# Optimization experiments

Hardware: AMD Instinct MI355X
Metric: run time of the kernel (lower is better)

## Reference

```python
import jax, jax.numpy as jnp
import numpy as np

N_QUBITS = 8
D_K = 64
B, S = 8, 1024


def _single_qubit_states(xang, theta):
    # xang: [B,S,n] values in [-1,1] (post-tanh); theta: [n,3] Rot params (phi, theta, omega)
    # state = RZ(omega) @ RY(th) @ RZ(phi) @ RY(pi*xang) |0>
    a = xang * jnp.pi
    c = jnp.cos(a * 0.5)          # [B,S,n]
    s = jnp.sin(a * 0.5)
    phi, th, om = theta[:, 0], theta[:, 1], theta[:, 2]   # each [n]
    ct = jnp.cos(th * 0.5)
    st = jnp.sin(th * 0.5)
    e_mpo = jnp.exp(-0.5j * (phi + om))   # e^{-i(phi+omega)/2}
    e_pmo = jnp.exp(0.5j * (phi - om))    # e^{+i(phi-omega)/2}
    amp0 = e_mpo * ct * c - e_pmo * st * s
    amp1 = jnp.conj(e_pmo) * st * c + jnp.conj(e_mpo) * ct * s
    return jnp.stack([amp0, amp1], axis=-1)   # [B,S,n,2] complex64


def setup_inputs() -> dict:
    key = jax.random.key(0)
    k1, k2, k3, k4 = jax.random.split(key, 4)
    x = jax.random.normal(k1, (B, S, D_K), dtype=jnp.float32)
    theta_q = jax.random.normal(k2, (N_QUBITS, 3), dtype=jnp.float32) * 0.1
    theta_k = jax.random.normal(k3, (N_QUBITS, 3), dtype=jnp.float32) * 0.1
    W_v = jax.random.normal(k4, (D_K, D_K), dtype=jnp.float32) / np.sqrt(D_K)
    b_v = jnp.zeros((D_K,), dtype=jnp.float32)
    return {"x": x, "theta_q": theta_q, "theta_k": theta_k, "W_v": W_v, "b_v": b_v}


def reference(x, theta_q, theta_k, W_v, b_v):
    n = theta_q.shape[0]
    xn = jnp.tanh(x[..., :n])                 # [B,S,n]
    qs = _single_qubit_states(xn, theta_q)    # [B,S,n,2]
    ks = _single_qubit_states(xn, theta_k)    # [B,S,n,2]
    # per-qubit overlap <q_i | k_j> for every (b, s, t) pair
    ov = jnp.einsum('bsnc,btnc->bstn', jnp.conj(qs), ks)  # [B,S,S,n] complex
    mag2 = jnp.real(ov) ** 2 + jnp.imag(ov) ** 2
    core = jnp.prod(mag2, axis=-1)            # |<psi_q|psi_k>|^2 = swap-test <Z>
    scores = (core + 1.0) * 0.5               # [B,S,S]
    attn = jax.nn.softmax(scores, axis=-1)
    values = x @ W_v.T + b_v                  # [B,S,D]
    out = jnp.einsum('bst,btd->bsd', attn, values)
    return out, attn
```

## Files before the change

### kernel.cpp

```cpp
#include <hip/hip_runtime.h>
#include <hip/hip_fp16.h>
#include <math.h>

#define NQ 8
#define DK 64
#define NB 8
#define NS 1024
#define RB 8
#define EPITCH 1032

typedef _Float16 h2v __attribute__((ext_vector_type(2)));

__device__ __forceinline__ float fdot2h(unsigned qu, unsigned ku, float acc) {
#if defined(__has_builtin) && __has_builtin(__builtin_amdgcn_fdot2)
    union { unsigned u; h2v h; } a, b;
    a.u = qu; b.u = ku;
    return __builtin_amdgcn_fdot2(a.h, b.h, acc, false);
#else
    __half2 qh = *(__half2*)&qu, kh = *(__half2*)&ku;
    float2 qf = __half22float2(qh), kf = __half22float2(kh);
    return fmaf(qf.x, kf.x, fmaf(qf.y, kf.y, acc));
#endif
}

__global__ __launch_bounds__(256) void prep_kernel(
    const float* __restrict__ x,
    const float* __restrict__ theta_q,
    const float* __restrict__ theta_k,
    const float* __restrict__ Wv,
    const float* __restrict__ bv,
    __half* __restrict__ qdh, __half* __restrict__ kdh,
    __half* __restrict__ v2) {
    int bid = blockIdx.x;
    int tid = threadIdx.x;
    if (bid < 2048) {
        int t = bid * 4 + (tid >> 6);
        int d = tid & 63;
        const float4* xr = (const float4*)(x + (size_t)t * DK);
        const float4* wr = (const float4*)(Wv + (size_t)d * DK);
        float a0 = bv[d], a1 = 0.f, a2 = 0.f, a3 = 0.f;
#pragma unroll
        for (int j = 0; j < DK / 4; ++j) {
            float4 xv = xr[j], wv = wr[j];
            a0 = fmaf(xv.x, wv.x, a0);
            a1 = fmaf(xv.y, wv.y, a1);
            a2 = fmaf(xv.z, wv.z, a2);
            a3 = fmaf(xv.w, wv.w, a3);
        }
        float v = (a0 + a1) + (a2 + a3);
        int b = t >> 10, ti = t & 1023;
        v2[((size_t)(b * 512 + (ti >> 1)) * 64 + d) * 2 + (ti & 1)] = __float2half_rn(v);
    } else {
        __shared__ float tt[2][NQ][6];
        if (tid < 16) {
            int side = tid >> 3, n = tid & 7;
            const float* thp = side ? theta_k : theta_q;
            float phi = thp[n * 3 + 0], th = thp[n * 3 + 1], om = thp[n * 3 + 2];
            float st, ct; __sincosf(0.5f * th, &st, &ct);
            float smpo, cmpo; __sincosf(0.5f * (phi + om), &smpo, &cmpo);
            float spmo, cpmo; __sincosf(0.5f * (phi - om), &spmo, &cpmo);
            tt[side][n][0] = ct;  tt[side][n][1] = st;
            tt[side][n][2] = cmpo; tt[side][n][3] = smpo;
            tt[side][n][4] = cpmo; tt[side][n][5] = spmo;
        }
        __syncthreads();

        int gid = (bid - 2048) * 256 + tid;
        int tok = gid >> 3;
        int n = gid & 7;
        float xin = x[(size_t)tok * DK + n];
        float ex = __expf(2.0f * xin);
        float xn = 1.0f - 2.0f / (ex + 1.0f);
        float s, c;
        __sincosf(xn * 1.57079632679489662f, &s, &c);

#pragma unroll
        for (int side = 0; side < 2; ++side) {
            float ct = tt[side][n][0], st = tt[side][n][1];
            float cmpo = tt[side][n][2], smpo = tt[side][n][3];
            float cpmo = tt[side][n][4], spmo = tt[side][n][5];
            float a = ct * c, b2 = st * s, cc = st * c, d2 = ct * s;
            float a0re =  cmpo * a - cpmo * b2;
            float a0im = -smpo * a - spmo * b2;
            float a1re =  cpmo * cc + cmpo * d2;
            float a1im = -spmo * cc + smpo * d2;
            float d0 = fmaf(a0re, a0re, a0im * a0im);
            float d1 = fmaf(a1re, a1re, a1im * a1im);
            float ur = fmaf(a1re, a0re, a1im * a0im);
            float ui = fmaf(a1im, a0re, -a1re * a0im);
            if (side == 0) {
                __half2* qp = (__half2*)(qdh + (size_t)tok * 32 + n * 4);
                qp[0] = __floats2half2_rn(d0, d1);
                qp[1] = __floats2half2_rn(ur, ui);
            } else {
                __half2* kp = (__half2*)(kdh + (size_t)tok * 32 + n * 4);
                kp[0] = __floats2half2_rn(d0, d1);
                kp[1] = __floats2half2_rn(2.f * ur, 2.f * ui);
            }
        }
    }
}

__global__ __launch_bounds__(256, 4) void attn_kernel(
    const __half* __restrict__ qdh, const __half* __restrict__ kdh,
    const __half* __restrict__ v2,
    float* __restrict__ out, float* __restrict__ attn) {
    __shared__ __align__(16) unsigned char smem[RB * EPITCH * 2];
    __half (*e16)[EPITCH] = (__half(*)[EPITCH])smem;
    float* red = (float*)smem;
    __shared__ float red_lds[4][RB];
    __shared__ float inv_lds[RB];

    int tid = threadIdx.x;
    int gr0 = blockIdx.x * RB;
    int b = gr0 >> 10;
    int w = tid >> 6, lane = tid & 63;

    const __half* kfb = kdh + (size_t)b * NS * 32;

    int t0 = w * 256;
    uint4 kv[4][4];
#pragma unroll
    for (int j = 0; j < 4; ++j) {
        const uint4* kp = (const uint4*)(kfb + (size_t)(t0 + j * 64 + lane) * 32);
        kv[j][0] = kp[0]; kv[j][1] = kp[1]; kv[j][2] = kp[2]; kv[j][3] = kp[3];
    }

    float sums[RB];
#pragma unroll
    for (int r = 0; r < RB; ++r) sums[r] = 0.f;

#pragma unroll
    for (int r = 0; r < RB; ++r) {
        const unsigned* qp = (const unsigned*)(qdh + (size_t)(gr0 + r) * 32);
        unsigned sq[16];
#pragma unroll
        for (int i = 0; i < 16; ++i) sq[i] = __builtin_amdgcn_readfirstlane(qp[i]);
#pragma unroll
        for (int j = 0; j < 4; ++j) {
            float m0 = fdot2h(sq[ 0], kv[j][0].x, fdot2h(sq[ 1], kv[j][0].y, 0.f));
            float m1 = fdot2h(sq[ 2], kv[j][0].z, fdot2h(sq[ 3], kv[j][0].w, 0.f));
            float m2 = fdot2h(sq[ 4], kv[j][1].x, fdot2h(sq[ 5], kv[j][1].y, 0.f));
            float m3 = fdot2h(sq[ 6], kv[j][1].z, fdot2h(sq[ 7], kv[j][1].w, 0.f));
            float m4 = fdot2h(sq[ 8], kv[j][2].x, fdot2h(sq[ 9], kv[j][2].y, 0.f));
            float m5 = fdot2h(sq[10], kv[j][2].z, fdot2h(sq[11], kv[j][2].w, 0.f));
            float m6 = fdot2h(sq[12], kv[j][3].x, fdot2h(sq[13], kv[j][3].y, 0.f));
            float m7 = fdot2h(sq[14], kv[j][3].z, fdot2h(sq[15], kv[j][3].w, 0.f));
            float core = ((m0 * m1) * (m2 * m3)) * ((m4 * m5) * (m6 * m7));
            float e = __expf(fmaf(core, 0.5f, 0.5f));
            e16[r][t0 + j * 64 + lane] = __float2half_rn(e);
            sums[r] += e;
        }
    }

#pragma unroll
    for (int r = 0; r < RB; ++r) {
#pragma unroll
        for (int m = 1; m < 64; m <<= 1) sums[r] += __shfl_xor(sums[r], m, 64);
    }
    if (lane == 0) {
#pragma unroll
        for (int r = 0; r < RB; ++r) red_lds[w][r] = sums[r];
    }
    __syncthreads();
    if (tid < RB)
        inv_lds[tid] = 1.f / (red_lds[0][tid] + red_lds[1][tid] + red_lds[2][tid] + red_lds[3][tid]);
    __syncthreads();

    float* ab = attn + (size_t)gr0 * NS;
#pragma unroll
    for (int r = 0; r < RB; ++r) {
        float iv = inv_lds[r];
        uint2 raw = *(const uint2*)&e16[r][tid * 4];
        __half2* hp = (__half2*)&raw;
        float2 lo = __half22float2(hp[0]), hi = __half22float2(hp[1]);
        *(float4*)&ab[(size_t)r * NS + tid * 4] =
            make_float4(lo.x * iv, lo.y * iv, hi.x * iv, hi.y * iv);
    }

    int tg = tid >> 4, dg = tid & 15;
    const __half* v2b = v2 + (size_t)b * 512 * 128;
    float acc[RB][4];
#pragma unroll
    for (int r = 0; r < RB; ++r) { acc[r][0] = acc[r][1] = acc[r][2] = acc[r][3] = 0.f; }

    for (int jj = 0; jj < 32; ++jj) {
        int p = jj * 16 + tg;
        uint4 vv = *(const uint4*)(v2b + (size_t)p * 128 + dg * 8);
        unsigned ep[RB];
#pragma unroll
        for (int r = 0; r < RB; ++r) ep[r] = *(const unsigned*)&e16[r][2 * p];
#pragma unroll
        for (int r = 0; r < RB; ++r) {
            acc[r][0] = fdot2h(ep[r], vv.x, acc[r][0]);
            acc[r][1] = fdot2h(ep[r], vv.y, acc[r][1]);
            acc[r][2] = fdot2h(ep[r], vv.z, acc[r][2]);
            acc[r][3] = fdot2h(ep[r], vv.w, acc[r][3]);
        }
    }

#pragma unroll
    for (int h = 0; h < 2; ++h) {
        __syncthreads();
#pragma unroll
        for (int r = 0; r < 4; ++r) {
            *(float4*)&red[((size_t)tg * 4 + r) * 64 + dg * 4] =
                make_float4(acc[h * 4 + r][0], acc[h * 4 + r][1],
                            acc[h * 4 + r][2], acc[h * 4 + r][3]);
        }
        __syncthreads();
        int r2 = tid >> 6, d = tid & 63;
        float o = 0.f;
#pragma unroll
        for (int g = 0; g < 16; ++g) o += red[((size_t)g * 4 + r2) * 64 + d];
        out[((size_t)(gr0 + h * 4 + r2)) * DK + d] = o * inv_lds[h * 4 + r2];
    }
}

extern "C" void kernel_launch(void* const* d_in, const int* in_sizes, int n_in,
                              void* d_out, int out_size, void* d_ws, size_t ws_size,
                              hipStream_t stream) {
    const float* x       = (const float*)d_in[0];
    const float* theta_q = (const float*)d_in[1];
    const float* theta_k = (const float*)d_in[2];
    const float* W_v     = (const float*)d_in[3];
    const float* b_v     = (const float*)d_in[4];

    float* out  = (float*)d_out;
    float* attn = (float*)d_out + (size_t)NB * NS * DK;

    __half* qdh = (__half*)d_ws;
    __half* kdh = qdh + (size_t)NB * NS * 32;
    __half* v2  = kdh + (size_t)NB * NS * 32;

    prep_kernel<<<2048 + NB * NS * NQ / 256, 256, 0, stream>>>(
        x, theta_q, theta_k, W_v, b_v, qdh, kdh, v2);
    attn_kernel<<<NB * NS / RB, 256, 0, stream>>>(qdh, kdh, v2, out, attn);
}
```

Measured before the change: 52.37 us.

## Fuse query state prep into attention kernel and pair tokens in value projection

The query density-matrix computation moves from the prep kernel into the attention kernel. Each block now builds the fp16 query terms for its 8 rows in shared memory, which removes the qdh workspace round trip. The value projection now computes two tokens per thread, so each W_v row is loaded once per pair and written as a single half2 store, and the block count drops by half. The V loop in the attention kernel prefetches the next vector before the dot products, at the cost of an extra barrier and some redundant per-block trig work.

```diff
diff --git a/kernel.cpp b/kernel.cpp
--- a/kernel.cpp
+++ b/kernel.cpp
@@ -23,91 +23,93 @@
 #endif
 }
 
+__device__ __forceinline__ void qk_density(float s, float c,
+                                           const float* t6,
+                                           float& d0, float& d1, float& ur, float& ui) {
+    float ct = t6[0], st = t6[1], cmpo = t6[2], smpo = t6[3], cpmo = t6[4], spmo = t6[5];
+    float a = ct * c, b2 = st * s, cc = st * c, d2 = ct * s;
+    float a0re =  cmpo * a - cpmo * b2;
+    float a0im = -smpo * a - spmo * b2;
+    float a1re =  cpmo * cc + cmpo * d2;
+    float a1im = -spmo * cc + smpo * d2;
+    d0 = fmaf(a0re, a0re, a0im * a0im);
+    d1 = fmaf(a1re, a1re, a1im * a1im);
+    ur = fmaf(a1re, a0re, a1im * a0im);
+    ui = fmaf(a1im, a0re, -a1re * a0im);
+}
+
+__device__ __forceinline__ void theta_table(const float* __restrict__ thp, int n, float* t6) {
+    float phi = thp[n * 3 + 0], th = thp[n * 3 + 1], om = thp[n * 3 + 2];
+    float st, ct; __sincosf(0.5f * th, &st, &ct);
+    float smpo, cmpo; __sincosf(0.5f * (phi + om), &smpo, &cmpo);
+    float spmo, cpmo; __sincosf(0.5f * (phi - om), &spmo, &cpmo);
+    t6[0] = ct; t6[1] = st; t6[2] = cmpo; t6[3] = smpo; t6[4] = cpmo; t6[5] = spmo;
+}
+
+__device__ __forceinline__ void tanh_sincos(float xin, float& s, float& c) {
+    float ex = __expf(2.0f * xin);
+    float xn = 1.0f - 2.0f / (ex + 1.0f);
+    __sincosf(xn * 1.57079632679489662f, &s, &c);
+}
+
 __global__ __launch_bounds__(256) void prep_kernel(
     const float* __restrict__ x,
-    const float* __restrict__ theta_q,
     const float* __restrict__ theta_k,
     const float* __restrict__ Wv,
     const float* __restrict__ bv,
-    __half* __restrict__ qdh, __half* __restrict__ kdh,
+    __half* __restrict__ kdh,
     __half* __restrict__ v2) {
     int bid = blockIdx.x;
     int tid = threadIdx.x;
-    if (bid < 2048) {
-        int t = bid * 4 + (tid >> 6);
+    if (bid < 1024) {
+        int gp = bid * 4 + (tid >> 6);
         int d = tid & 63;
-        const float4* xr = (const float4*)(x + (size_t)t * DK);
+        int t0 = gp * 2;
+        const float4* x0 = (const float4*)(x + (size_t)t0 * DK);
+        const float4* x1 = (const float4*)(x + (size_t)(t0 + 1) * DK);
         const float4* wr = (const float4*)(Wv + (size_t)d * DK);
-        float a0 = bv[d], a1 = 0.f, a2 = 0.f, a3 = 0.f;
+        float p0 = bv[d], p1 = bv[d], q0 = 0.f, q1 = 0.f;
 #pragma unroll
         for (int j = 0; j < DK / 4; ++j) {
-            float4 xv = xr[j], wv = wr[j];
-            a0 = fmaf(xv.x, wv.x, a0);
-            a1 = fmaf(xv.y, wv.y, a1);
-            a2 = fmaf(xv.z, wv.z, a2);
-            a3 = fmaf(xv.w, wv.w, a3);
-        }
-        float v = (a0 + a1) + (a2 + a3);
-        int b = t >> 10, ti = t & 1023;
-        v2[((size_t)(b * 512 + (ti >> 1)) * 64 + d) * 2 + (ti & 1)] = __float2half_rn(v);
+            float4 wv = wr[j];
+            float4 a = x0[j], b = x1[j];
+            p0 = fmaf(a.x, wv.x, p0); q0 = fmaf(a.y, wv.y, q0);
+            p0 = fmaf(a.z, wv.z, p0); q0 = fmaf(a.w, wv.w, q0);
+            p1 = fmaf(b.x, wv.x, p1); q1 = fmaf(b.y, wv.y, q1);
+            p1 = fmaf(b.z, wv.z, p1); q1 = fmaf(b.w, wv.w, q1);
+        }
+        int b = t0 >> 10, pi = (t0 & 1023) >> 1;
+        __half2 hv = __floats2half2_rn(p0 + q0, p1 + q1);
+        *(__half2*)&v2[((size_t)(b * 512 + pi) * 64 + d) * 2] = hv;
     } else {
-        __shared__ float tt[2][NQ][6];
-        if (tid < 16) {
-            int side = tid >> 3, n = tid & 7;
-            const float* thp = side ? theta_k : theta_q;
-            float phi = thp[n * 3 + 0], th = thp[n * 3 + 1], om = thp[n * 3 + 2];
-            float st, ct; __sincosf(0.5f * th, &st, &ct);
-            float smpo, cmpo; __sincosf(0.5f * (phi + om), &smpo, &cmpo);
-            float spmo, cpmo; __sincosf(0.5f * (phi - om), &spmo, &cpmo);
-            tt[side][n][0] = ct;  tt[side][n][1] = st;
-            tt[side][n][2] = cmpo; tt[side][n][3] = smpo;
-            tt[side][n][4] = cpmo; tt[side][n][5] = spmo;
-        }
+        __shared__ float tk[NQ][6];
+        if (tid < NQ) theta_table(theta_k, tid, tk[tid]);
         __syncthreads();
 
-        int gid = (bid - 2048) * 256 + tid;
+        int gid = (bid - 1024) * 256 + tid;
         int tok = gid >> 3;
         int n = gid & 7;
-        float xin = x[(size_t)tok * DK + n];
-        float ex = __expf(2.0f * xin);
-        float xn = 1.0f - 2.0f / (ex + 1.0f);
         float s, c;
-        __sincosf(xn * 1.57079632679489662f, &s, &c);
-
-#pragma unroll
-        for (int side = 0; side < 2; ++side) {
-            float ct = tt[side][n][0], st = tt[side][n][1];
-            float cmpo = tt[side][n][2], smpo = tt[side][n][3];
-            float cpmo = tt[side][n][4], spmo = tt[side][n][5];
-            float a = ct * c, b2 = st * s, cc = st * c, d2 = ct * s;
-            float a0re =  cmpo * a - cpmo * b2;
-            float a0im = -smpo * a - spmo * b2;
-            float a1re =  cpmo * cc + cmpo * d2;
-            float a1im = -spmo * cc + smpo * d2;
-            float d0 = fmaf(a0re, a0re, a0im * a0im);
-            float d1 = fmaf(a1re, a1re, a1im * a1im);
-            float ur = fmaf(a1re, a0re, a1im * a0im);
-            float ui = fmaf(a1im, a0re, -a1re * a0im);
-            if (side == 0) {
-                __half2* qp = (__half2*)(qdh + (size_t)tok * 32 + n * 4);
-                qp[0] = __floats2half2_rn(d0, d1);
-                qp[1] = __floats2half2_rn(ur, ui);
-            } else {
-                __half2* kp = (__half2*)(kdh + (size_t)tok * 32 + n * 4);
-                kp[0] = __floats2half2_rn(d0, d1);
-                kp[1] = __floats2half2_rn(2.f * ur, 2.f * ui);
-            }
-        }
+        tanh_sincos(x[(size_t)tok * DK + n], s, c);
+        float d0, d1, ur, ui;
+        qk_density(s, c, tk[n], d0, d1, ur, ui);
+        __half2* kp = (__half2*)(kdh + (size_t)tok * 32 + n * 4);
+        kp[0] = __floats2half2_rn(d0, d1);
+        kp[1] = __floats2half2_rn(2.f * ur, 2.f * ui);
     }
 }
 
 __global__ __launch_bounds__(256, 4) void attn_kernel(
-    const __half* __restrict__ qdh, const __half* __restrict__ kdh,
+    const float* __restrict__ x,
+    const float* __restrict__ theta_q,
+    const __half* __restrict__ kdh,
     const __half* __restrict__ v2,
     float* __restrict__ out, float* __restrict__ attn) {
     __shared__ __align__(16) unsigned char smem[RB * EPITCH * 2];
     __half (*e16)[EPITCH] = (__half(*)[EPITCH])smem;
     float* red = (float*)smem;
+    __shared__ unsigned q16[RB][16];
+    __shared__ float tq[NQ][6];
     __shared__ float red_lds[4][RB];
     __shared__ float inv_lds[RB];
 
@@ -116,8 +118,21 @@
     int b = gr0 >> 10;
     int w = tid >> 6, lane = tid & 63;
 
+    if (tid < NQ) theta_table(theta_q, tid, tq[tid]);
+    __syncthreads();
+    if (tid < RB * NQ) {
+        int r = tid >> 3, n = tid & 7;
+        float s, c;
+        tanh_sincos(x[(size_t)(gr0 + r) * DK + n], s, c);
+        float d0, d1, ur, ui;
+        qk_density(s, c, tq[n], d0, d1, ur, ui);
+        __half2 h0 = __floats2half2_rn(d0, d1);
+        __half2 h1 = __floats2half2_rn(ur, ui);
+        q16[r][2 * n + 0] = *(unsigned*)&h0;
+        q16[r][2 * n + 1] = *(unsigned*)&h1;
+    }
+
     const __half* kfb = kdh + (size_t)b * NS * 32;
-
     int t0 = w * 256;
     uint4 kv[4][4];
 #pragma unroll
@@ -125,6 +140,7 @@
         const uint4* kp = (const uint4*)(kfb + (size_t)(t0 + j * 64 + lane) * 32);
         kv[j][0] = kp[0]; kv[j][1] = kp[1]; kv[j][2] = kp[2]; kv[j][3] = kp[3];
     }
+    __syncthreads();
 
     float sums[RB];
 #pragma unroll
@@ -132,10 +148,9 @@
 
 #pragma unroll
     for (int r = 0; r < RB; ++r) {
-        const unsigned* qp = (const unsigned*)(qdh + (size_t)(gr0 + r) * 32);
         unsigned sq[16];
 #pragma unroll
-        for (int i = 0; i < 16; ++i) sq[i] = __builtin_amdgcn_readfirstlane(qp[i]);
+        for (int i = 0; i < 16; ++i) sq[i] = __builtin_amdgcn_readfirstlane(q16[r][i]);
 #pragma unroll
         for (int j = 0; j < 4; ++j) {
             float m0 = fdot2h(sq[ 0], kv[j][0].x, fdot2h(sq[ 1], kv[j][0].y, 0.f));
@@ -179,14 +194,16 @@
     }
 
     int tg = tid >> 4, dg = tid & 15;
-    const __half* v2b = v2 + (size_t)b * 512 * 128;
+    const __half* v2l = v2 + (size_t)b * 512 * 128 + dg * 8;
     float acc[RB][4];
 #pragma unroll
     for (int r = 0; r < RB; ++r) { acc[r][0] = acc[r][1] = acc[r][2] = acc[r][3] = 0.f; }
 
+    uint4 vv = *(const uint4*)(v2l + (size_t)tg * 128);
     for (int jj = 0; jj < 32; ++jj) {
         int p = jj * 16 + tg;
-        uint4 vv = *(const uint4*)(v2b + (size_t)p * 128 + dg * 8);
+        int pn = (jj < 31) ? p + 16 : p;
+        uint4 nxt = *(const uint4*)(v2l + (size_t)pn * 128);
         unsigned ep[RB];
 #pragma unroll
         for (int r = 0; r < RB; ++r) ep[r] = *(const unsigned*)&e16[r][2 * p];
@@ -197,6 +214,7 @@
             acc[r][2] = fdot2h(ep[r], vv.z, acc[r][2]);
             acc[r][3] = fdot2h(ep[r], vv.w, acc[r][3]);
         }
+        vv = nxt;
     }
 
 #pragma unroll
@@ -229,11 +247,10 @@
     float* out  = (float*)d_out;
     float* attn = (float*)d_out + (size_t)NB * NS * DK;
 
-    __half* qdh = (__half*)d_ws;
-    __half* kdh = qdh + (size_t)NB * NS * 32;
+    __half* kdh = (__half*)d_ws;
     __half* v2  = kdh + (size_t)NB * NS * 32;
 
-    prep_kernel<<<2048 + NB * NS * NQ / 256, 256, 0, stream>>>(
-        x, theta_q, theta_k, W_v, b_v, qdh, kdh, v2);
-    attn_kernel<<<NB * NS / RB, 256, 0, stream>>>(qdh, kdh, v2, out, attn);
-}
+    prep_kernel<<<1024 + NB * NS * NQ / 256, 256, 0, stream>>>(
+        x, theta_k, W_v, b_v, kdh, v2);
+    attn_kernel<<<NB * NS / RB, 256, 0, stream>>>(x, theta_q, kdh, v2, out, attn);
+}
```

New measurement: 51.97 us. About the same (-0.8%).
